# Kernel optimization log

Measured on AMD Instinct MI355X. Metric: run time of the kernel, lower is better.

## Reference

```python
import jax, jax.numpy as jnp
import numpy as np

N = 100_000      # nodes
E = 1_600_000    # edges (before self loops)
IN, HID, OUT, H = 128, 32, 40, 4
NEG_SLOPE = 0.2  # PyG GATConv default


def setup_inputs() -> dict:
    key = jax.random.key(0)
    ks = jax.random.split(key, 10)
    s = 0.1  # small init scale (glorot-like)
    return {
        "x": jax.random.normal(ks[0], (N, IN), jnp.float32),
        "edge_index": jax.random.randint(ks[1], (2, E), 0, N, dtype=jnp.int32),
        "W1": jax.random.normal(ks[2], (IN, H * HID), jnp.float32) * s,
        "att_src1": jax.random.normal(ks[3], (H, HID), jnp.float32) * s,
        "att_dst1": jax.random.normal(ks[4], (H, HID), jnp.float32) * s,
        "b1": jnp.zeros((H * HID,), jnp.float32),
        "W2": jax.random.normal(ks[5], (H * HID, H * OUT), jnp.float32) * s,
        "att_src2": jax.random.normal(ks[6], (H, OUT), jnp.float32) * s,
        "att_dst2": jax.random.normal(ks[7], (H, OUT), jnp.float32) * s,
        "b2": jnp.zeros((OUT,), jnp.float32),
    }


def gat_layer(x, src, dst, W, a_src, a_dst, b, concat):
    """PyG-style GATConv: edge (src -> dst), softmax over incoming edges per dst."""
    Hh, C = a_src.shape
    h = (x @ W).reshape(-1, Hh, C)                      # [N, H, C]
    s_src = jnp.einsum('nhc,hc->nh', h, a_src)           # [N, H]
    s_dst = jnp.einsum('nhc,hc->nh', h, a_dst)           # [N, H]
    e = jax.nn.leaky_relu(s_src[src] + s_dst[dst], NEG_SLOPE)  # [E', H]
    m = jax.ops.segment_max(e, dst, num_segments=N)      # per-dst max for stability
    p = jnp.exp(e - m[dst])
    z = jax.ops.segment_sum(p, dst, num_segments=N)
    alpha = p / z[dst]                                    # segment softmax [E', H]
    out = jax.ops.segment_sum(alpha[:, :, None] * h[src], dst, num_segments=N)  # [N,H,C]
    out = out.reshape(-1, Hh * C) if concat else out.mean(axis=1)
    return out + b


def reference(x, edge_index, W1, att_src1, att_dst1, b1, W2, att_src2, att_dst2, b2):
    loops = jnp.arange(N, dtype=edge_index.dtype)        # PyG add_self_loops=True
    src = jnp.concatenate([edge_index[0], loops])
    dst = jnp.concatenate([edge_index[1], loops])
    h = jax.nn.elu(gat_layer(x, src, dst, W1, att_src1, att_dst1, b1, concat=True))
    h = gat_layer(h, src, dst, W2, att_src2, att_dst2, b2, concat=False)
    return jax.nn.log_softmax(h, axis=1)
```

## Files before the change

kernel.cpp:

```cpp
#include <hip/hip_runtime.h>
#include <hip/hip_bf16.h>

#define N_NODES 100000
#define M_PAD   100096
#define N_EDGES 1600000
#define E_TOT   (N_EDGES + N_NODES)
#define NEG_SLOPE 0.2f

#define G_NODES 128
#define BUCKETS ((N_NODES + G_NODES - 1) / G_NODES)
#define REP 512
#define SLICE ((E_TOT + REP - 1) / REP)

typedef __attribute__((ext_vector_type(8))) short s16x8;
typedef __attribute__((ext_vector_type(4))) float f32x4;
typedef __attribute__((ext_vector_type(2))) float f32x2;

__device__ __forceinline__ float lo16(unsigned u) { return __uint_as_float(u << 16); }
__device__ __forceinline__ float hi16(unsigned u) { return __uint_as_float(u & 0xffff0000u); }

__device__ __forceinline__ short f2bf(float f) {
    __hip_bfloat16 b = __float2bfloat16(f);
    return *(short*)&b;
}


__global__ __launch_bounds__(256) void slice_count_kernel(const int* __restrict__ ei,
                                                          int* __restrict__ cnt) {
    __shared__ int h[BUCKETS];
    for (int i = threadIdx.x; i < BUCKETS; i += 256) h[i] = 0;
    __syncthreads();
    int r = blockIdx.x;
    int lo = r * SLICE, hi = min(lo + SLICE, E_TOT);
    for (int e = lo + threadIdx.x; e < hi; e += 256) {
        int d = (e < N_EDGES) ? ei[N_EDGES + e] : e - N_EDGES;
        atomicAdd(&h[d >> 7], 1);
    }
    __syncthreads();
    for (int i = threadIdx.x; i < BUCKETS; i += 256)
        cnt[(size_t)r * BUCKETS + i] = h[i];
}

__global__ __launch_bounds__(REP) void col_scan_kernel(int* __restrict__ cnt,
                                                       int* __restrict__ bsum) {
    __shared__ int lds[REP];
    int b = blockIdx.x, tid = threadIdx.x;
    int v = cnt[(size_t)tid * BUCKETS + b];
    lds[tid] = v;
    __syncthreads();
    for (int off = 1; off < REP; off <<= 1) {
        int t = (tid >= off) ? lds[tid - off] : 0;
        __syncthreads();
        lds[tid] += t;
        __syncthreads();
    }
    cnt[(size_t)tid * BUCKETS + b] = lds[tid] - v;
    if (tid == REP - 1) bsum[b] = lds[tid];
}

__global__ __launch_bounds__(1024) void bucket_scan_kernel(const int* __restrict__ bsum,
                                                           int* __restrict__ boff) {
    __shared__ int lds[1024];
    int tid = threadIdx.x;
    int v = (tid < BUCKETS) ? bsum[tid] : 0;
    lds[tid] = v;
    __syncthreads();
    for (int off = 1; off < 1024; off <<= 1) {
        int t = (tid >= off) ? lds[tid - off] : 0;
        __syncthreads();
        lds[tid] += t;
        __syncthreads();
    }
    if (tid < BUCKETS) boff[tid] = lds[tid] - v;
    if (tid == 0) boff[BUCKETS] = E_TOT;
}

__global__ __launch_bounds__(256) void bucket_scatter_kernel(const int* __restrict__ ei,
                                                             const int* __restrict__ colx,
                                                             const int* __restrict__ boff,
                                                             int* __restrict__ tmp) {
    __shared__ int lcur[BUCKETS];
    int r = blockIdx.x;
    for (int i = threadIdx.x; i < BUCKETS; i += 256)
        lcur[i] = boff[i] + colx[(size_t)r * BUCKETS + i];
    __syncthreads();
    int lo = r * SLICE, hi = min(lo + SLICE, E_TOT);
    for (int e = lo + threadIdx.x; e < hi; e += 256) {
        int s, d;
        if (e < N_EDGES) { s = ei[e]; d = ei[N_EDGES + e]; }
        else             { s = d = e - N_EDGES; }
        int pos = atomicAdd(&lcur[d >> 7], 1);
        tmp[pos] = (s << 7) | (d & (G_NODES - 1));
    }
}

__global__ __launch_bounds__(256) void bucket_build_kernel(const int* __restrict__ tmp,
                                                           const int* __restrict__ boff,
                                                           int* __restrict__ rowptr,
                                                           int* __restrict__ csr) {
    __shared__ int hcnt[G_NODES];
    __shared__ int hoff[G_NODES];
    int b = blockIdx.x;
    int base = boff[b], cnt = boff[b + 1] - base;
    int tid = threadIdx.x;
    if (tid < G_NODES) hcnt[tid] = 0;
    __syncthreads();
    for (int i = tid; i < cnt; i += 256)
        atomicAdd(&hcnt[tmp[base + i] & (G_NODES - 1)], 1);
    __syncthreads();
    if (tid < G_NODES) hoff[tid] = hcnt[tid];
    __syncthreads();
    for (int off = 1; off < G_NODES; off <<= 1) {
        int t = (tid < G_NODES && tid >= off) ? hoff[tid - off] : 0;
        __syncthreads();
        if (tid < G_NODES) hoff[tid] += t;
        __syncthreads();
    }
    if (tid < G_NODES) {
        int excl = hoff[tid] - hcnt[tid];
        int node = b * G_NODES + tid;
        if (node < N_NODES) rowptr[node] = base + excl;
        hcnt[tid] = excl;
    }
    __syncthreads();
    for (int i = tid; i < cnt; i += 256) {
        int v = tmp[base + i];
        int pos = base + atomicAdd(&hcnt[v & (G_NODES - 1)], 1);
        csr[pos] = v >> 7;
    }
    if (b == 0 && tid == 0) rowptr[N_NODES] = E_TOT;
}


__global__ void cvt_w_kernel(const float* __restrict__ W1, __hip_bfloat16* __restrict__ W1t,
                             const float* __restrict__ W2, __hip_bfloat16* __restrict__ W2t) {
    int idx = blockIdx.x * blockDim.x + threadIdx.x;
    if (idx < 128 * 128) {
        int k = idx >> 7, n = idx & 127;
        W1t[n * 128 + k] = __float2bfloat16(W1[idx]);
    } else if (idx < 128 * 128 + 128 * 160) {
        int i = idx - 128 * 128;
        int k = i / 160, n = i - k * 160;
        W2t[n * 128 + k] = __float2bfloat16(W2[i]);
    }
}


template<int NCOLS>
__global__ __launch_bounds__(256) void mfma_gemm_f32a_kernel(const float* __restrict__ A,
                                                             const __hip_bfloat16* __restrict__ Bt,
                                                             unsigned char* __restrict__ Cq) {
    constexpr int CG = NCOLS / 32;
    int wid = threadIdx.x >> 6;
    int lane = threadIdx.x & 63;
    int wr = wid >> 1, wc = wid & 1;
    int l15 = lane & 15, lk = lane >> 4;

    s16x8 bfrag[CG][4];
    #pragma unroll
    for (int cg = 0; cg < CG; ++cg) {
        int col = wc * (NCOLS / 2) + cg * 16 + l15;
        #pragma unroll
        for (int ks = 0; ks < 4; ++ks)
            bfrag[cg][ks] = *(const s16x8*)&Bt[col * 128 + ks * 32 + lk * 8];
    }
    int rowblk = blockIdx.x * 128;
    #pragma unroll
    for (int st = 0; st < 4; ++st) {
        int rbase = rowblk + st * 32 + wr * 16;
        int row = rbase + l15;
        bool ok = row < N_NODES;
        s16x8 afrag[4];
        #pragma unroll
        for (int ks = 0; ks < 4; ++ks) {
            if (ok) {
                float4 a0 = *(const float4*)&A[(size_t)row * 128 + ks * 32 + lk * 8];
                float4 a1 = *(const float4*)&A[(size_t)row * 128 + ks * 32 + lk * 8 + 4];
                s16x8 af;
                af[0] = f2bf(a0.x); af[1] = f2bf(a0.y); af[2] = f2bf(a0.z); af[3] = f2bf(a0.w);
                af[4] = f2bf(a1.x); af[5] = f2bf(a1.y); af[6] = f2bf(a1.z); af[7] = f2bf(a1.w);
                afrag[ks] = af;
            } else {
                afrag[ks] = (s16x8){0,0,0,0,0,0,0,0};
            }
        }
        f32x4 acc[CG];
        #pragma unroll
        for (int cg = 0; cg < CG; ++cg) acc[cg] = (f32x4){0.f, 0.f, 0.f, 0.f};
        #pragma unroll
        for (int ks = 0; ks < 4; ++ks) {
            #pragma unroll
            for (int cg = 0; cg < CG; ++cg)
                acc[cg] = __builtin_amdgcn_mfma_f32_16x16x32_bf16(afrag[ks], bfrag[cg][ks], acc[cg], 0, 0, 0);
        }
        #pragma unroll
        for (int cg = 0; cg < CG; ++cg) {
            int c = wc * (NCOLS / 2) + cg * 16 + l15;
            unsigned w01 = __builtin_amdgcn_cvt_pk_fp8_f32(acc[cg][0], acc[cg][1], 0, false);
            unsigned w23 = __builtin_amdgcn_cvt_pk_fp8_f32(acc[cg][2], acc[cg][3], 0, false);
            size_t base = (size_t)(rbase + lk * 4) * NCOLS + c;
            Cq[base]             = (unsigned char)(w01 & 0xff);
            Cq[base + NCOLS]     = (unsigned char)((w01 >> 8) & 0xff);
            Cq[base + 2 * NCOLS] = (unsigned char)(w23 & 0xff);
            Cq[base + 3 * NCOLS] = (unsigned char)((w23 >> 8) & 0xff);
        }
    }
}


template<int NCOLS>
__global__ __launch_bounds__(256) void mfma_gemm_kernel(const __hip_bfloat16* __restrict__ A,
                                                        const __hip_bfloat16* __restrict__ Bt,
                                                        unsigned char* __restrict__ Cq) {
    constexpr int CG = NCOLS / 32;
    int wid = threadIdx.x >> 6;
    int lane = threadIdx.x & 63;
    int wr = wid >> 1, wc = wid & 1;
    int l15 = lane & 15, lk = lane >> 4;

    s16x8 bfrag[CG][4];
    #pragma unroll
    for (int cg = 0; cg < CG; ++cg) {
        int col = wc * (NCOLS / 2) + cg * 16 + l15;
        #pragma unroll
        for (int ks = 0; ks < 4; ++ks)
            bfrag[cg][ks] = *(const s16x8*)&Bt[col * 128 + ks * 32 + lk * 8];
    }
    int rowblk = blockIdx.x * 128;
    #pragma unroll
    for (int st = 0; st < 4; ++st) {
        int rbase = rowblk + st * 32 + wr * 16;
        s16x8 afrag[4];
        #pragma unroll
        for (int ks = 0; ks < 4; ++ks)
            afrag[ks] = *(const s16x8*)&A[(size_t)(rbase + l15) * 128 + ks * 32 + lk * 8];
        f32x4 acc[CG];
        #pragma unroll
        for (int cg = 0; cg < CG; ++cg) acc[cg] = (f32x4){0.f, 0.f, 0.f, 0.f};
        #pragma unroll
        for (int ks = 0; ks < 4; ++ks) {
            #pragma unroll
            for (int cg = 0; cg < CG; ++cg)
                acc[cg] = __builtin_amdgcn_mfma_f32_16x16x32_bf16(afrag[ks], bfrag[cg][ks], acc[cg], 0, 0, 0);
        }
        #pragma unroll
        for (int cg = 0; cg < CG; ++cg) {
            int c = wc * (NCOLS / 2) + cg * 16 + l15;
            unsigned w01 = __builtin_amdgcn_cvt_pk_fp8_f32(acc[cg][0], acc[cg][1], 0, false);
            unsigned w23 = __builtin_amdgcn_cvt_pk_fp8_f32(acc[cg][2], acc[cg][3], 0, false);
            size_t base = (size_t)(rbase + lk * 4) * NCOLS + c;
            Cq[base]             = (unsigned char)(w01 & 0xff);
            Cq[base + NCOLS]     = (unsigned char)((w01 >> 8) & 0xff);
            Cq[base + 2 * NCOLS] = (unsigned char)(w23 & 0xff);
            Cq[base + 3 * NCOLS] = (unsigned char)((w23 >> 8) & 0xff);
        }
    }
}


template<int C, int J>
__global__ void score_fp8_kernel(const unsigned char* __restrict__ hq,
                                 const float* __restrict__ att_src,
                                 const float* __restrict__ att_dst,
                                 float* __restrict__ s_src, float* __restrict__ s_dst, int n) {
    int idx = blockIdx.x * blockDim.x + threadIdx.x;
    if (idx >= n * 4) return;
    int node = idx >> 2, hd = idx & 3;
    const unsigned char* hp = hq + (size_t)node * J + hd * C;
    const float* as = att_src + hd * C;
    const float* ad = att_dst + hd * C;
    float ss = 0.f, sd = 0.f;
    #pragma unroll
    for (int c8 = 0; c8 < C / 8; ++c8) {
        uint2 u = *(const uint2*)&hp[c8 * 8];
        f32x2 v0 = __builtin_amdgcn_cvt_pk_f32_fp8(u.x, false);
        f32x2 v1 = __builtin_amdgcn_cvt_pk_f32_fp8(u.x, true);
        f32x2 v2 = __builtin_amdgcn_cvt_pk_f32_fp8(u.y, false);
        f32x2 v3 = __builtin_amdgcn_cvt_pk_f32_fp8(u.y, true);
        int c = c8 * 8;
        ss += v0.x * as[c]     + v0.y * as[c + 1] + v1.x * as[c + 2] + v1.y * as[c + 3]
            + v2.x * as[c + 4] + v2.y * as[c + 5] + v3.x * as[c + 6] + v3.y * as[c + 7];
        sd += v0.x * ad[c]     + v0.y * ad[c + 1] + v1.x * ad[c + 2] + v1.y * ad[c + 3]
            + v2.x * ad[c + 4] + v2.y * ad[c + 5] + v3.x * ad[c + 6] + v3.y * ad[c + 7];
    }
    s_src[idx] = ss;
    s_dst[idx] = sd;
}


__global__ __launch_bounds__(256) void agg1_kernel(
        const unsigned char* __restrict__ h1q, const float* __restrict__ s_src,
        const float* __restrict__ s_dst, const int* __restrict__ rowptr,
        const int* __restrict__ csr, const float* __restrict__ b1,
        __hip_bfloat16* __restrict__ out1) {
    int d = blockIdx.x * 4 + (threadIdx.x >> 6);
    if (d >= N_NODES) return;
    int lane = threadIdx.x & 63;
    int c0 = lane * 2;
    int hd = lane >> 4;
    int bp = hd << 2;
    int eg = (lane >> 2) & 7;
    float sdall = s_dst[d * 4 + (lane & 3)];
    f32x2 acc = {0.f, 0.f};
    float z = 0.f;
    int beg = __builtin_amdgcn_readfirstlane(rowptr[d]);
    int end = __builtin_amdgcn_readfirstlane(rowptr[d + 1]);
    for (int j = beg; j < end; j += 8) {
        int cnt = end - j;
        int se = csr[min(j + eg, end - 1)];
        float ee = s_src[(size_t)se * 4 + (lane & 3)] + sdall;
        ee = fmaxf(ee, NEG_SLOPE * ee);
        float qv = (eg < cnt) ? __expf(ee) : 0.f;
        int qbits = __float_as_int(qv);
        #pragma unroll
        for (int t = 0; t < 8; ++t) {
            float q = __int_as_float(__builtin_amdgcn_ds_bpermute(bp + t * 16, qbits));
            int s = __builtin_amdgcn_readfirstlane(csr[min(j + t, end - 1)]);
            const unsigned char* row = h1q + (size_t)s * 128;
            unsigned u = *(const unsigned short*)&row[c0];
            f32x2 v = __builtin_amdgcn_cvt_pk_f32_fp8(u, false);
            f32x2 qq = {q, q};
            acc += qq * v;
            z += q;
        }
    }
    float invz = 1.0f / z;
    float vx = acc.x * invz + b1[c0];
    float vy = acc.y * invz + b1[c0 + 1];
    vx = vx > 0.f ? vx : __expf(vx) - 1.0f;
    vy = vy > 0.f ? vy : __expf(vy) - 1.0f;
    __hip_bfloat162 o;
    o.x = __float2bfloat16(vx);
    o.y = __float2bfloat16(vy);
    *(__hip_bfloat162*)&out1[(size_t)d * 128 + c0] = o;
}


__global__ __launch_bounds__(256) void agg2_kernel(
        const unsigned char* __restrict__ h2q, const float* __restrict__ s_src,
        const float* __restrict__ s_dst, const int* __restrict__ rowptr,
        const int* __restrict__ csr, const float* __restrict__ b2,
        float* __restrict__ out) {
    int d = blockIdx.x * 4 + (threadIdx.x >> 6);
    if (d >= N_NODES) return;
    int lane = threadIdx.x & 63;
    int ll = lane < 40 ? lane : 39;
    int hd = ll / 10;
    int bp = hd << 2;
    int eg = (lane >> 2) & 7;
    int voff = ll * 4;
    float sdall = s_dst[d * 4 + (lane & 3)];
    f32x2 acc01 = {0.f, 0.f}, acc23 = {0.f, 0.f};
    float z = 0.f;
    int beg = __builtin_amdgcn_readfirstlane(rowptr[d]);
    int end = __builtin_amdgcn_readfirstlane(rowptr[d + 1]);
    for (int j = beg; j < end; j += 8) {
        int cnt = end - j;
        int se = csr[min(j + eg, end - 1)];
        float ee = s_src[(size_t)se * 4 + (lane & 3)] + sdall;
        ee = fmaxf(ee, NEG_SLOPE * ee);
        float qv = (eg < cnt) ? __expf(ee) : 0.f;
        int qbits = __float_as_int(qv);
        #pragma unroll
        for (int t = 0; t < 8; ++t) {
            float q = __int_as_float(__builtin_amdgcn_ds_bpermute(bp + t * 16, qbits));
            int s = __builtin_amdgcn_readfirstlane(csr[min(j + t, end - 1)]);
            const unsigned char* row = h2q + (size_t)s * 160;
            unsigned u = *(const unsigned*)&row[voff];
            f32x2 v01 = __builtin_amdgcn_cvt_pk_f32_fp8(u, false);
            f32x2 v23 = __builtin_amdgcn_cvt_pk_f32_fp8(u, true);
            f32x2 qq = {q, q};
            acc01 += qq * v01;
            acc23 += qq * v23;
            z += q;
        }
    }
    float invz = 1.0f / z;
    float rx = acc01.x * invz, ry = acc01.y * invz;
    float rz = acc23.x * invz, rw = acc23.y * invz;
    float sx = rx + __shfl(rx, lane + 10) + __shfl(rx, lane + 20) + __shfl(rx, lane + 30);
    float sy = ry + __shfl(ry, lane + 10) + __shfl(ry, lane + 20) + __shfl(ry, lane + 30);
    float sz = rz + __shfl(rz, lane + 10) + __shfl(rz, lane + 20) + __shfl(rz, lane + 30);
    float sw = rw + __shfl(rw, lane + 10) + __shfl(rw, lane + 20) + __shfl(rw, lane + 30);
    int lc = lane < 10 ? lane : 9;
    float4 bb = *(const float4*)&b2[lc * 4];
    bool own = lane < 10;
    float vx = own ? sx * 0.25f + bb.x : -1e30f;
    float vy = own ? sy * 0.25f + bb.y : -1e30f;
    float vz = own ? sz * 0.25f + bb.z : -1e30f;
    float vw = own ? sw * 0.25f + bb.w : -1e30f;
    float m = fmaxf(fmaxf(vx, vy), fmaxf(vz, vw));
    #pragma unroll
    for (int off = 1; off < 16; off <<= 1) m = fmaxf(m, __shfl_xor(m, off));
    float ssum = 0.f;
    if (own) {
        ssum = __expf(vx - m) + __expf(vy - m) + __expf(vz - m) + __expf(vw - m);
    }
    #pragma unroll
    for (int off = 1; off < 16; off <<= 1) ssum += __shfl_xor(ssum, off);
    float lse = m + __logf(ssum);
    if (own) {
        float4 o = {vx - lse, vy - lse, vz - lse, vw - lse};
        *(float4*)&out[(size_t)d * 40 + lane * 4] = o;
    }
}


extern "C" void kernel_launch(void* const* d_in, const int* in_sizes, int n_in,
                              void* d_out, int out_size, void* d_ws, size_t ws_size,
                              hipStream_t stream) {
    const float* x   = (const float*)d_in[0];
    const int*   ei  = (const int*)d_in[1];
    const float* W1  = (const float*)d_in[2];
    const float* as1 = (const float*)d_in[3];
    const float* ad1 = (const float*)d_in[4];
    const float* b1  = (const float*)d_in[5];
    const float* W2  = (const float*)d_in[6];
    const float* as2 = (const float*)d_in[7];
    const float* ad2 = (const float*)d_in[8];
    const float* b2  = (const float*)d_in[9];
    float* out = (float*)d_out;

    char* ws = (char*)d_ws;
    size_t off = 0;
    auto alloc = [&](size_t bytes) {
        void* p = ws + off;
        off += (bytes + 255) & ~(size_t)255;
        return p;
    };
    unsigned char*  h1q   = (unsigned char*)alloc((size_t)M_PAD * 128);
    unsigned char*  h2q   = (unsigned char*)alloc((size_t)M_PAD * 160);
    __hip_bfloat16* out1b = (__hip_bfloat16*)alloc((size_t)M_PAD * 128 * 2);
    __hip_bfloat16* W1t   = (__hip_bfloat16*)alloc((size_t)128 * 128 * 2);
    __hip_bfloat16* W2t   = (__hip_bfloat16*)alloc((size_t)160 * 128 * 2);
    float* s_src1  = (float*)alloc((size_t)N_NODES * 4 * 4);
    float* s_dst1  = (float*)alloc((size_t)N_NODES * 4 * 4);
    float* s_src2  = (float*)alloc((size_t)N_NODES * 4 * 4);
    float* s_dst2  = (float*)alloc((size_t)N_NODES * 4 * 4);
    int*   tmp     = (int*)alloc((size_t)E_TOT * 4);
    int*   rowptr  = (int*)alloc((size_t)(N_NODES + 1) * 4);
    int*   csr     = (int*)alloc((size_t)E_TOT * 4);
    int*   cnt     = (int*)alloc((size_t)REP * BUCKETS * 4);
    int*   bsum    = (int*)alloc((size_t)BUCKETS * 4);
    int*   boff    = (int*)alloc((size_t)(BUCKETS + 1) * 4);

    slice_count_kernel<<<REP, 256, 0, stream>>>(ei, cnt);
    col_scan_kernel<<<BUCKETS, REP, 0, stream>>>(cnt, bsum);
    bucket_scan_kernel<<<1, 1024, 0, stream>>>(bsum, boff);
    bucket_scatter_kernel<<<REP, 256, 0, stream>>>(ei, cnt, boff, tmp);
    bucket_build_kernel<<<BUCKETS, 256, 0, stream>>>(tmp, boff, rowptr, csr);

    cvt_w_kernel<<<(128 * 128 + 128 * 160 + 255) / 256, 256, 0, stream>>>(W1, W1t, W2, W2t);

    mfma_gemm_f32a_kernel<128><<<M_PAD / 128, 256, 0, stream>>>(x, W1t, h1q);
    score_fp8_kernel<32, 128><<<(N_NODES * 4 + 255) / 256, 256, 0, stream>>>(h1q, as1, ad1, s_src1, s_dst1, N_NODES);
    agg1_kernel<<<(N_NODES + 3) / 4, 256, 0, stream>>>(h1q, s_src1, s_dst1, rowptr, csr, b1, out1b);

    mfma_gemm_kernel<160><<<M_PAD / 128, 256, 0, stream>>>(out1b, W2t, h2q);
    score_fp8_kernel<40, 160><<<(N_NODES * 4 + 255) / 256, 256, 0, stream>>>(h2q, as2, ad2, s_src2, s_dst2, N_NODES);
    agg2_kernel<<<(N_NODES + 3) / 4, 256, 0, stream>>>(h2q, s_src2, s_dst2, rowptr, csr, b2, out);
}
```

Before: 249.9 us.

## Gather eight edges per wave step with wide row loads in GAT aggregation

Both aggregation kernels change how work is mapped to lanes. Each group of 8 lanes now handles one edge and loads 16 or 20 contiguous bytes of the source row, so a wave covers 8 edges per iteration instead of walking them one at a time with scalar-broadcast indices and 2 to 4 byte loads. Per-edge partial sums are combined with cross-lane xor shuffles and then redistributed through shared memory before the bias, activation and output stages. This removes the serial inner loop and uses wider gathers, at the cost of more accumulator registers, a shuffle reduction and an LDS round trip per node.

```diff
diff --git a/kernel.cpp b/kernel.cpp
--- a/kernel.cpp
+++ b/kernel.cpp
@@ -293,46 +293,74 @@
         const float* __restrict__ s_dst, const int* __restrict__ rowptr,
         const int* __restrict__ csr, const float* __restrict__ b1,
         __hip_bfloat16* __restrict__ out1) {
-    int d = blockIdx.x * 4 + (threadIdx.x >> 6);
+    __shared__ float red[4][128];
+    int w = threadIdx.x >> 6;
+    int d = blockIdx.x * 4 + w;
     if (d >= N_NODES) return;
     int lane = threadIdx.x & 63;
-    int c0 = lane * 2;
-    int hd = lane >> 4;
-    int bp = hd << 2;
-    int eg = (lane >> 2) & 7;
-    float sdall = s_dst[d * 4 + (lane & 3)];
-    f32x2 acc = {0.f, 0.f};
-    float z = 0.f;
+    int g  = lane >> 3;
+    int sl = lane & 7;
+    int e  = (lane >> 2) & 7;
+    int hh = lane & 3;
+    int bpq = g * 16 + (sl >> 1) * 4;
+    float sd_h = s_dst[d * 4 + hh];
+    f32x2 acc[8];
+    #pragma unroll
+    for (int k = 0; k < 8; ++k) acc[k] = (f32x2){0.f, 0.f};
+    float zacc = 0.f;
     int beg = __builtin_amdgcn_readfirstlane(rowptr[d]);
     int end = __builtin_amdgcn_readfirstlane(rowptr[d + 1]);
     for (int j = beg; j < end; j += 8) {
         int cnt = end - j;
-        int se = csr[min(j + eg, end - 1)];
-        float ee = s_src[(size_t)se * 4 + (lane & 3)] + sdall;
+        int se = csr[min(j + e, end - 1)];
+        float ee = s_src[(size_t)se * 4 + hh] + sd_h;
         ee = fmaxf(ee, NEG_SLOPE * ee);
-        float qv = (eg < cnt) ? __expf(ee) : 0.f;
-        int qbits = __float_as_int(qv);
-        #pragma unroll
-        for (int t = 0; t < 8; ++t) {
-            float q = __int_as_float(__builtin_amdgcn_ds_bpermute(bp + t * 16, qbits));
-            int s = __builtin_amdgcn_readfirstlane(csr[min(j + t, end - 1)]);
-            const unsigned char* row = h1q + (size_t)s * 128;
-            unsigned u = *(const unsigned short*)&row[c0];
-            f32x2 v = __builtin_amdgcn_cvt_pk_f32_fp8(u, false);
-            f32x2 qq = {q, q};
-            acc += qq * v;
-            z += q;
-        }
-    }
-    float invz = 1.0f / z;
-    float vx = acc.x * invz + b1[c0];
-    float vy = acc.y * invz + b1[c0 + 1];
+        float qv = (e < cnt) ? __expf(ee) : 0.f;
+        zacc += qv;
+        float q = __int_as_float(__builtin_amdgcn_ds_bpermute(bpq, __float_as_int(qv)));
+        int s = csr[min(j + g, end - 1)];
+        const unsigned char* row = h1q + (size_t)s * 128 + sl * 16;
+        uint4 u = *(const uint4*)row;
+        f32x2 qq = {q, q};
+        acc[0] += qq * __builtin_amdgcn_cvt_pk_f32_fp8(u.x, false);
+        acc[1] += qq * __builtin_amdgcn_cvt_pk_f32_fp8(u.x, true);
+        acc[2] += qq * __builtin_amdgcn_cvt_pk_f32_fp8(u.y, false);
+        acc[3] += qq * __builtin_amdgcn_cvt_pk_f32_fp8(u.y, true);
+        acc[4] += qq * __builtin_amdgcn_cvt_pk_f32_fp8(u.z, false);
+        acc[5] += qq * __builtin_amdgcn_cvt_pk_f32_fp8(u.z, true);
+        acc[6] += qq * __builtin_amdgcn_cvt_pk_f32_fp8(u.w, false);
+        acc[7] += qq * __builtin_amdgcn_cvt_pk_f32_fp8(u.w, true);
+    }
+    #pragma unroll
+    for (int k = 0; k < 8; ++k) {
+        float a0 = acc[k].x, a1 = acc[k].y;
+        a0 += __shfl_xor(a0, 8);  a1 += __shfl_xor(a1, 8);
+        a0 += __shfl_xor(a0, 16); a1 += __shfl_xor(a1, 16);
+        a0 += __shfl_xor(a0, 32); a1 += __shfl_xor(a1, 32);
+        acc[k].x = a0; acc[k].y = a1;
+    }
+    zacc += __shfl_xor(zacc, 4);
+    zacc += __shfl_xor(zacc, 8);
+    zacc += __shfl_xor(zacc, 16);
+    float zh = __int_as_float(__builtin_amdgcn_ds_bpermute((sl >> 1) * 4, __float_as_int(zacc)));
+    float invz = 1.0f / zh;
+    if (g == 0) {
+        #pragma unroll
+        for (int k = 0; k < 8; ++k) {
+            red[w][sl * 16 + k * 2]     = acc[k].x * invz;
+            red[w][sl * 16 + k * 2 + 1] = acc[k].y * invz;
+        }
+    }
+    asm volatile("s_waitcnt lgkmcnt(0)" ::: "memory");
+    float2 v2 = *(float2*)&red[w][lane * 2];
+    float vx = v2.x + b1[lane * 2];
+    float vy = v2.y + b1[lane * 2 + 1];
     vx = vx > 0.f ? vx : __expf(vx) - 1.0f;
     vy = vy > 0.f ? vy : __expf(vy) - 1.0f;
     __hip_bfloat162 o;
     o.x = __float2bfloat16(vx);
     o.y = __float2bfloat16(vy);
-    *(__hip_bfloat162*)&out1[(size_t)d * 128 + c0] = o;
+    *(__hip_bfloat162*)&out1[(size_t)d * 128 + lane * 2] = o;
 }
 
 
@@ -341,43 +369,71 @@
         const float* __restrict__ s_dst, const int* __restrict__ rowptr,
         const int* __restrict__ csr, const float* __restrict__ b2,
         float* __restrict__ out) {
-    int d = blockIdx.x * 4 + (threadIdx.x >> 6);
+    __shared__ float red[4][160];
+    int w = threadIdx.x >> 6;
+    int d = blockIdx.x * 4 + w;
     if (d >= N_NODES) return;
     int lane = threadIdx.x & 63;
-    int ll = lane < 40 ? lane : 39;
-    int hd = ll / 10;
-    int bp = hd << 2;
-    int eg = (lane >> 2) & 7;
-    int voff = ll * 4;
-    float sdall = s_dst[d * 4 + (lane & 3)];
-    f32x2 acc01 = {0.f, 0.f}, acc23 = {0.f, 0.f};
-    float z = 0.f;
+    int g  = lane >> 3;
+    int sl = lane & 7;
+    int e  = (lane >> 2) & 7;
+    int hh = lane & 3;
+    int bpq = g * 16 + (sl >> 1) * 4;
+    float sd_h = s_dst[d * 4 + hh];
+    f32x2 acc[10];
+    #pragma unroll
+    for (int k = 0; k < 10; ++k) acc[k] = (f32x2){0.f, 0.f};
+    float zacc = 0.f;
     int beg = __builtin_amdgcn_readfirstlane(rowptr[d]);
     int end = __builtin_amdgcn_readfirstlane(rowptr[d + 1]);
     for (int j = beg; j < end; j += 8) {
         int cnt = end - j;
-        int se = csr[min(j + eg, end - 1)];
-        float ee = s_src[(size_t)se * 4 + (lane & 3)] + sdall;
+        int se = csr[min(j + e, end - 1)];
+        float ee = s_src[(size_t)se * 4 + hh] + sd_h;
         ee = fmaxf(ee, NEG_SLOPE * ee);
-        float qv = (eg < cnt) ? __expf(ee) : 0.f;
-        int qbits = __float_as_int(qv);
-        #pragma unroll
-        for (int t = 0; t < 8; ++t) {
-            float q = __int_as_float(__builtin_amdgcn_ds_bpermute(bp + t * 16, qbits));
-            int s = __builtin_amdgcn_readfirstlane(csr[min(j + t, end - 1)]);
-            const unsigned char* row = h2q + (size_t)s * 160;
-            unsigned u = *(const unsigned*)&row[voff];
-            f32x2 v01 = __builtin_amdgcn_cvt_pk_f32_fp8(u, false);
-            f32x2 v23 = __builtin_amdgcn_cvt_pk_f32_fp8(u, true);
-            f32x2 qq = {q, q};
-            acc01 += qq * v01;
-            acc23 += qq * v23;
-            z += q;
-        }
-    }
-    float invz = 1.0f / z;
-    float rx = acc01.x * invz, ry = acc01.y * invz;
-    float rz = acc23.x * invz, rw = acc23.y * invz;
+        float qv = (e < cnt) ? __expf(ee) : 0.f;
+        zacc += qv;
+        float q = __int_as_float(__builtin_amdgcn_ds_bpermute(bpq, __float_as_int(qv)));
+        int s = csr[min(j + g, end - 1)];
+        const unsigned char* row = h2q + (size_t)s * 160 + sl * 20;
+        uint4 u = *(const uint4*)row;
+        unsigned u4 = *(const unsigned*)(row + 16);
+        f32x2 qq = {q, q};
+        acc[0] += qq * __builtin_amdgcn_cvt_pk_f32_fp8(u.x, false);
+        acc[1] += qq * __builtin_amdgcn_cvt_pk_f32_fp8(u.x, true);
+        acc[2] += qq * __builtin_amdgcn_cvt_pk_f32_fp8(u.y, false);
+        acc[3] += qq * __builtin_amdgcn_cvt_pk_f32_fp8(u.y, true);
+        acc[4] += qq * __builtin_amdgcn_cvt_pk_f32_fp8(u.z, false);
+        acc[5] += qq * __builtin_amdgcn_cvt_pk_f32_fp8(u.z, true);
+        acc[6] += qq * __builtin_amdgcn_cvt_pk_f32_fp8(u.w, false);
+        acc[7] += qq * __builtin_amdgcn_cvt_pk_f32_fp8(u.w, true);
+        acc[8] += qq * __builtin_amdgcn_cvt_pk_f32_fp8(u4, false);
+        acc[9] += qq * __builtin_amdgcn_cvt_pk_f32_fp8(u4, true);
+    }
+    #pragma unroll
+    for (int k = 0; k < 10; ++k) {
+        float a0 = acc[k].x, a1 = acc[k].y;
+        a0 += __shfl_xor(a0, 8);  a1 += __shfl_xor(a1, 8);
+        a0 += __shfl_xor(a0, 16); a1 += __shfl_xor(a1, 16);
+        a0 += __shfl_xor(a0, 32); a1 += __shfl_xor(a1, 32);
+        acc[k].x = a0; acc[k].y = a1;
+    }
+    zacc += __shfl_xor(zacc, 4);
+    zacc += __shfl_xor(zacc, 8);
+    zacc += __shfl_xor(zacc, 16);
+    float zh = __int_as_float(__builtin_amdgcn_ds_bpermute((sl >> 1) * 4, __float_as_int(zacc)));
+    float invz = 1.0f / zh;
+    if (g == 0) {
+        #pragma unroll
+        for (int k = 0; k < 10; ++k) {
+            red[w][sl * 20 + k * 2]     = acc[k].x * invz;
+            red[w][sl * 20 + k * 2 + 1] = acc[k].y * invz;
+        }
+    }
+    asm volatile("s_waitcnt lgkmcnt(0)" ::: "memory");
+    int ll = lane < 40 ? lane : 39;
+    float4 rr = *(float4*)&red[w][ll * 4];
+    float rx = rr.x, ry = rr.y, rz = rr.z, rw = rr.w;
     float sx = rx + __shfl(rx, lane + 10) + __shfl(rx, lane + 20) + __shfl(rx, lane + 30);
     float sy = ry + __shfl(ry, lane + 10) + __shfl(ry, lane + 20) + __shfl(ry, lane + 30);
     float sz = rz + __shfl(rz, lane + 10) + __shfl(rz, lane + 20) + __shfl(rz, lane + 30);
```

Measured after the change: 299.2 us. 19.7% more time.

## Merge independent CSR-build and GEMM/score stages into shared multi-role kernels

Applied to the files above, without the earlier changes.

Packs independent work into combined launches: the slice count runs with the weight conversion, the column scan with the first GEMM, and the bucket scan with the first score pass, each dispatching on block index. The column scan now uses 256 threads with two elements per thread, so it fits the 256-thread launch. This cuts three kernel launches and lets the small CSR-preprocessing blocks overlap with the dense work. The costs are heavier block shapes, for example 1024-thread score blocks. The csr buffer also gains 8 zeroed padding entries, which are unused in the visible code.

```diff
diff --git a/kernel.cpp b/kernel.cpp
--- a/kernel.cpp
+++ b/kernel.cpp
@@ -11,6 +11,9 @@
 #define BUCKETS ((N_NODES + G_NODES - 1) / G_NODES)
 #define REP 512
 #define SLICE ((E_TOT + REP - 1) / REP)
+#define GB1 (M_PAD / 128)
+#define CVTW_ELEMS (128 * 128 + 128 * 160)
+#define CVTW_BLOCKS ((CVTW_ELEMS + 255) / 256)
 
 typedef __attribute__((ext_vector_type(8))) short s16x8;
 typedef __attribute__((ext_vector_type(4))) float f32x4;
@@ -25,12 +28,10 @@
 }
 
 
-__global__ __launch_bounds__(256) void slice_count_kernel(const int* __restrict__ ei,
-                                                          int* __restrict__ cnt) {
+__device__ void slice_count_body(const int* __restrict__ ei, int* __restrict__ cnt, int r) {
     __shared__ int h[BUCKETS];
     for (int i = threadIdx.x; i < BUCKETS; i += 256) h[i] = 0;
     __syncthreads();
-    int r = blockIdx.x;
     int lo = r * SLICE, hi = min(lo + SLICE, E_TOT);
     for (int e = lo + threadIdx.x; e < hi; e += 256) {
         int d = (e < N_EDGES) ? ei[N_EDGES + e] : e - N_EDGES;
@@ -41,25 +42,27 @@
         cnt[(size_t)r * BUCKETS + i] = h[i];
 }
 
-__global__ __launch_bounds__(REP) void col_scan_kernel(int* __restrict__ cnt,
-                                                       int* __restrict__ bsum) {
-    __shared__ int lds[REP];
-    int b = blockIdx.x, tid = threadIdx.x;
-    int v = cnt[(size_t)tid * BUCKETS + b];
-    lds[tid] = v;
-    __syncthreads();
-    for (int off = 1; off < REP; off <<= 1) {
+__device__ void col_scan256_body(int* __restrict__ cnt, int* __restrict__ bsum, int b) {
+    __shared__ int lds[256];
+    int tid = threadIdx.x;
+    int v0 = cnt[(size_t)(2 * tid) * BUCKETS + b];
+    int v1 = cnt[(size_t)(2 * tid + 1) * BUCKETS + b];
+    int s = v0 + v1;
+    lds[tid] = s;
+    __syncthreads();
+    for (int off = 1; off < 256; off <<= 1) {
         int t = (tid >= off) ? lds[tid - off] : 0;
         __syncthreads();
         lds[tid] += t;
         __syncthreads();
     }
-    cnt[(size_t)tid * BUCKETS + b] = lds[tid] - v;
-    if (tid == REP - 1) bsum[b] = lds[tid];
-}
-
-__global__ __launch_bounds__(1024) void bucket_scan_kernel(const int* __restrict__ bsum,
-                                                           int* __restrict__ boff) {
+    int excl = lds[tid] - s;
+    cnt[(size_t)(2 * tid) * BUCKETS + b]     = excl;
+    cnt[(size_t)(2 * tid + 1) * BUCKETS + b] = excl + v0;
+    if (tid == 255) bsum[b] = lds[255];
+}
+
+__device__ void bucket_scan_body(const int* __restrict__ bsum, int* __restrict__ boff) {
     __shared__ int lds[1024];
     int tid = threadIdx.x;
     int v = (tid < BUCKETS) ? bsum[tid] : 0;
@@ -128,28 +131,27 @@
         int pos = base + atomicAdd(&hcnt[v & (G_NODES - 1)], 1);
         csr[pos] = v >> 7;
     }
+    if (b == 0 && tid < 8) csr[E_TOT + tid] = 0;
     if (b == 0 && tid == 0) rowptr[N_NODES] = E_TOT;
 }
 
 
-__global__ void cvt_w_kernel(const float* __restrict__ W1, __hip_bfloat16* __restrict__ W1t,
-                             const float* __restrict__ W2, __hip_bfloat16* __restrict__ W2t) {
-    int idx = blockIdx.x * blockDim.x + threadIdx.x;
+__device__ void cvt_w_body(const float* __restrict__ W1, __hip_bfloat16* __restrict__ W1t,
+                           const float* __restrict__ W2, __hip_bfloat16* __restrict__ W2t,
+                           int idx) {
     if (idx < 128 * 128) {
         int k = idx >> 7, n = idx & 127;
         W1t[n * 128 + k] = __float2bfloat16(W1[idx]);
-    } else if (idx < 128 * 128 + 128 * 160) {
+    } else if (idx < CVTW_ELEMS) {
         int i = idx - 128 * 128;
         int k = i / 160, n = i - k * 160;
         W2t[n * 128 + k] = __float2bfloat16(W2[i]);
     }
 }
 
-
-template<int NCOLS>
-__global__ __launch_bounds__(256) void mfma_gemm_f32a_kernel(const float* __restrict__ A,
-                                                             const __hip_bfloat16* __restrict__ Bt,
-                                                             unsigned char* __restrict__ Cq) {
+__device__ void gemm1_body(const float* __restrict__ A, const __hip_bfloat16* __restrict__ Bt,
+                           unsigned char* __restrict__ Cq, int bid) {
+    constexpr int NCOLS = 128;
     constexpr int CG = NCOLS / 32;
     int wid = threadIdx.x >> 6;
     int lane = threadIdx.x & 63;
@@ -164,7 +166,7 @@
         for (int ks = 0; ks < 4; ++ks)
             bfrag[cg][ks] = *(const s16x8*)&Bt[col * 128 + ks * 32 + lk * 8];
     }
-    int rowblk = blockIdx.x * 128;
+    int rowblk = bid * 128;
     #pragma unroll
     for (int st = 0; st < 4; ++st) {
         int rbase = rowblk + st * 32 + wr * 16;
@@ -207,7 +209,6 @@
     }
 }
 
-
 template<int NCOLS>
 __global__ __launch_bounds__(256) void mfma_gemm_kernel(const __hip_bfloat16* __restrict__ A,
                                                         const __hip_bfloat16* __restrict__ Bt,
@@ -259,12 +260,11 @@
 
 
 template<int C, int J>
-__global__ void score_fp8_kernel(const unsigned char* __restrict__ hq,
-                                 const float* __restrict__ att_src,
-                                 const float* __restrict__ att_dst,
-                                 float* __restrict__ s_src, float* __restrict__ s_dst, int n) {
-    int idx = blockIdx.x * blockDim.x + threadIdx.x;
-    if (idx >= n * 4) return;
+__device__ void score_body(const unsigned char* __restrict__ hq,
+                           const float* __restrict__ att_src,
+                           const float* __restrict__ att_dst,
+                           float* __restrict__ s_src, float* __restrict__ s_dst, int idx) {
+    if (idx >= N_NODES * 4) return;
     int node = idx >> 2, hd = idx & 3;
     const unsigned char* hp = hq + (size_t)node * J + hd * C;
     const float* as = att_src + hd * C;
@@ -285,6 +285,47 @@
     }
     s_src[idx] = ss;
     s_dst[idx] = sd;
+}
+
+template<int C, int J>
+__global__ void score_fp8_kernel(const unsigned char* __restrict__ hq,
+                                 const float* __restrict__ att_src,
+                                 const float* __restrict__ att_dst,
+                                 float* __restrict__ s_src, float* __restrict__ s_dst) {
+    score_body<C, J>(hq, att_src, att_dst, s_src, s_dst,
+                     blockIdx.x * blockDim.x + threadIdx.x);
+}
+
+
+__global__ __launch_bounds__(256) void k0_slice_cvtw(const int* __restrict__ ei,
+                                                     int* __restrict__ cnt,
+                                                     const float* __restrict__ W1,
+                                                     __hip_bfloat16* __restrict__ W1t,
+                                                     const float* __restrict__ W2,
+                                                     __hip_bfloat16* __restrict__ W2t) {
+    if (blockIdx.x < REP) { slice_count_body(ei, cnt, blockIdx.x); return; }
+    cvt_w_body(W1, W1t, W2, W2t, (blockIdx.x - REP) * 256 + threadIdx.x);
+}
+
+__global__ __launch_bounds__(256) void k1_colscan_gemm1(int* __restrict__ cnt,
+                                                        int* __restrict__ bsum,
+                                                        const float* __restrict__ A,
+                                                        const __hip_bfloat16* __restrict__ Bt,
+                                                        unsigned char* __restrict__ Cq) {
+    if (blockIdx.x < BUCKETS) { col_scan256_body(cnt, bsum, blockIdx.x); return; }
+    gemm1_body(A, Bt, Cq, blockIdx.x - BUCKETS);
+}
+
+__global__ __launch_bounds__(1024) void k2_bscan_score1(const int* __restrict__ bsum,
+                                                        int* __restrict__ boff,
+                                                        const unsigned char* __restrict__ h1q,
+                                                        const float* __restrict__ as1,
+                                                        const float* __restrict__ ad1,
+                                                        float* __restrict__ s_src1,
+                                                        float* __restrict__ s_dst1) {
+    if (blockIdx.x == 0) { bucket_scan_body(bsum, boff); return; }
+    score_body<32, 128>(h1q, as1, ad1, s_src1, s_dst1,
+                        (blockIdx.x - 1) * 1024 + threadIdx.x);
 }
 
 
@@ -334,7 +375,6 @@
     o.y = __float2bfloat16(vy);
     *(__hip_bfloat162*)&out1[(size_t)d * 128 + c0] = o;
 }
-
 
 __global__ __launch_bounds__(256) void agg2_kernel(
         const unsigned char* __restrict__ h2q, const float* __restrict__ s_src,
@@ -439,24 +479,21 @@
     float* s_dst2  = (float*)alloc((size_t)N_NODES * 4 * 4);
     int*   tmp     = (int*)alloc((size_t)E_TOT * 4);
     int*   rowptr  = (int*)alloc((size_t)(N_NODES + 1) * 4);
-    int*   csr     = (int*)alloc((size_t)E_TOT * 4);
+    int*   csr     = (int*)alloc((size_t)(E_TOT + 8) * 4);
     int*   cnt     = (int*)alloc((size_t)REP * BUCKETS * 4);
     int*   bsum    = (int*)alloc((size_t)BUCKETS * 4);
     int*   boff    = (int*)alloc((size_t)(BUCKETS + 1) * 4);
 
-    slice_count_kernel<<<REP, 256, 0, stream>>>(ei, cnt);
-    col_scan_kernel<<<BUCKETS, REP, 0, stream>>>(cnt, bsum);
-    bucket_scan_kernel<<<1, 1024, 0, stream>>>(bsum, boff);
+    k0_slice_cvtw<<<REP + CVTW_BLOCKS, 256, 0, stream>>>(ei, cnt, W1, W1t, W2, W2t);
+    k1_colscan_gemm1<<<BUCKETS + GB1, 256, 0, stream>>>(cnt, bsum, x, W1t, h1q);
+    k2_bscan_score1<<<1 + (N_NODES * 4 + 1023) / 1024, 1024, 0, stream>>>(
+        bsum, boff, h1q, as1, ad1, s_src1, s_dst1);
     bucket_scatter_kernel<<<REP, 256, 0, stream>>>(ei, cnt, boff, tmp);
     bucket_build_kernel<<<BUCKETS, 256, 0, stream>>>(tmp, boff, rowptr, csr);
 
-    cvt_w_kernel<<<(128 * 128 + 128 * 160 + 255) / 256, 256, 0, stream>>>(W1, W1t, W2, W2t);
-
-    mfma_gemm_f32a_kernel<128><<<M_PAD / 128, 256, 0, stream>>>(x, W1t, h1q);
-    score_fp8_kernel<32, 128><<<(N_NODES * 4 + 255) / 256, 256, 0, stream>>>(h1q, as1, ad1, s_src1, s_dst1, N_NODES);
     agg1_kernel<<<(N_NODES + 3) / 4, 256, 0, stream>>>(h1q, s_src1, s_dst1, rowptr, csr, b1, out1b);
 
-    mfma_gemm_kernel<160><<<M_PAD / 128, 256, 0, stream>>>(out1b, W2t, h2q);
-    score_fp8_kernel<40, 160><<<(N_NODES * 4 + 255) / 256, 256, 0, stream>>>(h2q, as2, ad2, s_src2, s_dst2, N_NODES);
+    mfma_gemm_kernel<160><<<GB1, 256, 0, stream>>>(out1b, W2t, h2q);
+    score_fp8_kernel<40, 160><<<(N_NODES * 4 + 255) / 256, 256, 0, stream>>>(h2q, as2, ad2, s_src2, s_dst2);
     agg2_kernel<<<(N_NODES + 3) / 4, 256, 0, stream>>>(h2q, s_src2, s_dst2, rowptr, csr, b2, out);
 }
```

New measurement: 242.1 us. 1.03x faster.
